# Kernel optimization log

Hardware: AMD Instinct MI355X
Metric: run time of the kernel (lower is better)

Reference implementation:

```python
import jax, jax.numpy as jnp
import numpy as np


def bilinear_sample(img, xs, ys):
    # img: [C,H,W]; xs, ys: [Ho,Wo] fractional source coords (pixel units).
    # Zero-fill outside the image, matching grid_sample(padding_mode='zeros').
    C, H, W = img.shape
    x0f = jnp.floor(xs); y0f = jnp.floor(ys)
    wx = xs - x0f; wy = ys - y0f
    x0 = x0f.astype(jnp.int32); y0 = y0f.astype(jnp.int32)

    def gather(yi, xi):
        inb = ((xi >= 0) & (xi <= W - 1) & (yi >= 0) & (yi <= H - 1))
        xc = jnp.clip(xi, 0, W - 1); yc = jnp.clip(yi, 0, H - 1)
        return img[:, yc, xc] * inb[None].astype(img.dtype)

    v00 = gather(y0,     x0)
    v01 = gather(y0,     x0 + 1)
    v10 = gather(y0 + 1, x0)
    v11 = gather(y0 + 1, x0 + 1)
    return (v00 * (1 - wx) * (1 - wy) + v01 * wx * (1 - wy)
            + v10 * (1 - wx) * wy + v11 * wx * wy)


def setup_inputs() -> dict:
    key = jax.random.key(0)
    k1, k2 = jax.random.split(key)
    frame = jax.random.uniform(k1, (1, 4, 1080, 1920), dtype=jnp.float32)
    # last channel is the alpha/transparency mask: fully opaque frame
    frame = frame.at[:, -1].set(1.0)
    canvas = jax.random.uniform(k2, (1, 4, 2048, 3072), dtype=jnp.float32)
    # realistic near-identity homography: small rotation + translation + tiny perspective
    th = 0.02
    Hmat = jnp.array([[np.cos(th), -np.sin(th), 400.0],
                      [np.sin(th),  np.cos(th), 300.0],
                      [1e-6,        0.0,        1.0]], dtype=jnp.float32)
    return {"frame": frame, "Hmat": Hmat, "canvas": canvas}


def reference(frame, Hmat, canvas):
    # Homography warp of `frame` into the canvas coordinate grid (inverse warp +
    # bilinear resample), then 'over' alpha-compositing onto the canvas
    # (merge_frame), fused into one pass over the canvas buffer.
    _, C, Hc, Wc = canvas.shape
    Hinv = jnp.linalg.inv(Hmat)
    dt = frame.dtype
    ys, xs = jnp.meshgrid(jnp.arange(Hc, dtype=dt), jnp.arange(Wc, dtype=dt), indexing='ij')
    coords = jnp.stack([xs, ys, jnp.ones_like(xs)])          # [3,Hc,Wc]
    src = jnp.einsum('ij,jhw->ihw', Hinv, coords)            # [3,Hc,Wc]
    sx = src[0] / src[2]
    sy = src[1] / src[2]
    warped = bilinear_sample(frame[0], sx, sy)               # [C,Hc,Wc]
    a_s = warped[-1:]                                        # source alpha
    a_c = canvas[0, -1:]                                     # canvas alpha
    out_rgb = warped[:-1] * a_s + canvas[0, :-1] * a_c * (1.0 - a_s)
    out_a = a_s + a_c * (1.0 - a_s)
    return jnp.concatenate([out_rgb, out_a], axis=0)[None]   # [1,C,Hc,Wc]
```

## Files before the change

kernel.cpp:

```cpp
#include <hip/hip_runtime.h>


#define FH 1080
#define FW 1920
#define CHh 2048
#define CWw 3072
#define FHW (FH * FW)
#define CHW (CHh * CWw)

__global__ __launch_bounds__(256) void interleave_kernel(
    const float* __restrict__ frame, float4* __restrict__ fi)
{
    const int idx = blockIdx.x * 256 + threadIdx.x;
    float4 v;
    v.x = frame[idx];
    v.y = frame[FHW + idx];
    v.z = frame[2 * FHW + idx];
    v.w = frame[3 * FHW + idx];
    fi[idx] = v;
}

__global__ __launch_bounds__(256) void pano1_kernel(
    const float4* __restrict__ fi,
    const float* __restrict__ Hm,
    const float* __restrict__ canvas,
    float* __restrict__ out)
{
    const int x = blockIdx.x * 256 + threadIdx.x;
    const int y = blockIdx.y;
    const int pix = y * CWw + x;

    const float a  = Hm[0], b  = Hm[1], c  = Hm[2];
    const float d  = Hm[3], e  = Hm[4], f  = Hm[5];
    const float g  = Hm[6], hh = Hm[7], i9 = Hm[8];
    const float A0 = e * i9 - f * hh, A1 = c * hh - b * i9, A2 = b * f - c * e;
    const float B0 = f * g  - d * i9, B1 = a * i9 - c * g,  B2 = c * d - a * f;
    const float C0 = d * hh - e * g,  C1 = b * g  - a * hh, C2 = a * e - b * d;

    const float xf = (float)x, yf = (float)y;
    const float u = fmaf(A0, xf, fmaf(A1, yf, A2));
    const float v = fmaf(B0, xf, fmaf(B1, yf, B2));
    const float w = fmaf(C0, xf, fmaf(C1, yf, C2));
    const float invw = __builtin_amdgcn_rcpf(w);
    const float sx = u * invw;
    const float sy = v * invw;

    const float x0f = floorf(sx);
    const float y0f = floorf(sy);
    const float wx = sx - x0f;
    const float wy = sy - y0f;
    const int x0 = (int)x0f;
    const int y0 = (int)y0f;

    const float c0 = canvas[0 * CHW + pix];
    const float c1 = canvas[1 * CHW + pix];
    const float c2 = canvas[2 * CHW + pix];
    const float ac = canvas[3 * CHW + pix];

    float wr = 0.f, wg = 0.f, wb = 0.f, wa = 0.f;

    if (x0 >= -1 && x0 <= FW - 1 && y0 >= -1 && y0 <= FH - 1) {
        const int x1 = x0 + 1, y1 = y0 + 1;
        const float mx0 = (x0 >= 0) ? 1.f : 0.f;
        const float mx1 = (x1 <= FW - 1) ? 1.f : 0.f;
        const float my0 = (y0 >= 0) ? 1.f : 0.f;
        const float my1 = (y1 <= FH - 1) ? 1.f : 0.f;
        const int xc0 = min(max(x0, 0), FW - 1);
        const int xc1 = min(max(x1, 0), FW - 1);
        const int yc0 = min(max(y0, 0), FH - 1);
        const int yc1 = min(max(y1, 0), FH - 1);

        const float w00 = (1.f - wx) * (1.f - wy) * mx0 * my0;
        const float w01 = wx * (1.f - wy) * mx1 * my0;
        const float w10 = (1.f - wx) * wy * mx0 * my1;
        const float w11 = wx * wy * mx1 * my1;

        const float4 v00 = fi[yc0 * FW + xc0];
        const float4 v01 = fi[yc0 * FW + xc1];
        const float4 v10 = fi[yc1 * FW + xc0];
        const float4 v11 = fi[yc1 * FW + xc1];

        wr = fmaf(w00, v00.x, fmaf(w01, v01.x, fmaf(w10, v10.x, w11 * v11.x)));
        wg = fmaf(w00, v00.y, fmaf(w01, v01.y, fmaf(w10, v10.y, w11 * v11.y)));
        wb = fmaf(w00, v00.z, fmaf(w01, v01.z, fmaf(w10, v10.z, w11 * v11.z)));
        wa = fmaf(w00, v00.w, fmaf(w01, v01.w, fmaf(w10, v10.w, w11 * v11.w)));
    }

    const float k = ac * (1.f - wa);
    out[0 * CHW + pix] = fmaf(wr, wa, c0 * k);
    out[1 * CHW + pix] = fmaf(wg, wa, c1 * k);
    out[2 * CHW + pix] = fmaf(wb, wa, c2 * k);
    out[3 * CHW + pix] = wa + k;
}

__global__ __launch_bounds__(256) void pano_kernel(
    const float* __restrict__ frame,
    const float* __restrict__ Hm,
    const float* __restrict__ canvas,
    float* __restrict__ out)
{
    const int x = blockIdx.x * 256 + threadIdx.x;
    const int y = blockIdx.y;
    const int pix = y * CWw + x;

    const float a  = Hm[0], b  = Hm[1], c  = Hm[2];
    const float d  = Hm[3], e  = Hm[4], f  = Hm[5];
    const float g  = Hm[6], hh = Hm[7], i9 = Hm[8];
    const float A0 = e * i9 - f * hh, A1 = c * hh - b * i9, A2 = b * f - c * e;
    const float B0 = f * g  - d * i9, B1 = a * i9 - c * g,  B2 = c * d - a * f;
    const float C0 = d * hh - e * g,  C1 = b * g  - a * hh, C2 = a * e - b * d;

    const float xf = (float)x, yf = (float)y;
    const float u = A0 * xf + A1 * yf + A2;
    const float v = B0 * xf + B1 * yf + B2;
    const float w = C0 * xf + C1 * yf + C2;
    const float sx = u / w;
    const float sy = v / w;

    const float x0f = floorf(sx);
    const float y0f = floorf(sy);
    const float wx = sx - x0f;
    const float wy = sy - y0f;
    const int x0 = (int)x0f;
    const int y0 = (int)y0f;

    const float c0 = canvas[0 * CHW + pix];
    const float c1 = canvas[1 * CHW + pix];
    const float c2 = canvas[2 * CHW + pix];
    const float ac = canvas[3 * CHW + pix];

    float w0 = 0.f, w1 = 0.f, w2 = 0.f, as = 0.f;
    if (x0 >= -1 && x0 <= FW - 1 && y0 >= -1 && y0 <= FH - 1) {
        const int x1 = x0 + 1, y1 = y0 + 1;
        const float mx0 = (x0 >= 0) ? 1.f : 0.f;
        const float mx1 = (x1 <= FW - 1) ? 1.f : 0.f;
        const float my0 = (y0 >= 0) ? 1.f : 0.f;
        const float my1 = (y1 <= FH - 1) ? 1.f : 0.f;
        const int xc0 = min(max(x0, 0), FW - 1);
        const int xc1 = min(max(x1, 0), FW - 1);
        const int yc0 = min(max(y0, 0), FH - 1);
        const int yc1 = min(max(y1, 0), FH - 1);

        const float w00 = (1.f - wx) * (1.f - wy) * mx0 * my0;
        const float w01 = wx * (1.f - wy) * mx1 * my0;
        const float w10 = (1.f - wx) * wy * mx0 * my1;
        const float w11 = wx * wy * mx1 * my1;

        const int i00 = yc0 * FW + xc0;
        const int i01 = yc0 * FW + xc1;
        const int i10 = yc1 * FW + xc0;
        const int i11 = yc1 * FW + xc1;

        #pragma unroll
        for (int chn = 0; chn < 4; ++chn) {
            const float* fp = frame + chn * FHW;
            const float val = w00 * fp[i00] + w01 * fp[i01]
                            + w10 * fp[i10] + w11 * fp[i11];
            if (chn == 0) w0 = val;
            else if (chn == 1) w1 = val;
            else if (chn == 2) w2 = val;
            else as = val;
        }
    }

    const float k = ac * (1.f - as);
    out[0 * CHW + pix] = w0 * as + c0 * k;
    out[1 * CHW + pix] = w1 * as + c1 * k;
    out[2 * CHW + pix] = w2 * as + c2 * k;
    out[3 * CHW + pix] = as + k;
}

extern "C" void kernel_launch(void* const* d_in, const int* in_sizes, int n_in,
                              void* d_out, int out_size, void* d_ws, size_t ws_size,
                              hipStream_t stream) {
    const float* frame  = (const float*)d_in[0];
    const float* Hm     = (const float*)d_in[1];
    const float* canvas = (const float*)d_in[2];
    float* out = (float*)d_out;

    const size_t need = (size_t)FHW * sizeof(float4);
    if (ws_size >= need) {
        float4* fi = (float4*)d_ws;
        interleave_kernel<<<dim3(FHW / 256), dim3(256), 0, stream>>>(frame, fi);
        pano1_kernel<<<dim3(CWw / 256, CHh), dim3(256), 0, stream>>>(fi, Hm, canvas, out);
    } else {
        pano_kernel<<<dim3(CWw / 256, CHh), dim3(256), 0, stream>>>(frame, Hm, canvas, out);
    }
}
```

Baseline: 207.1 us.

## Pack frame to fp16 and process two canvas pixels per thread

Replaces the float4 interleaved frame with a half-precision RGBA packed layout, fetching both horizontal bilinear neighbours with one 16-byte load per row. The main kernel now handles two adjacent canvas pixels per thread using float2 loads and stores. This shrinks the workspace and gather traffic and lowers per-pixel instruction overhead, at the cost of fp16 rounding of the source frame values.

```diff
diff --git a/kernel.cpp b/kernel.cpp
--- a/kernel.cpp
+++ b/kernel.cpp
@@ -1,4 +1,5 @@
 #include <hip/hip_runtime.h>
+#include <hip/hip_fp16.h>
 
 
 #define FH 1080
@@ -8,27 +9,42 @@
 #define FHW (FH * FW)
 #define CHW (CHh * CWw)
 
-__global__ __launch_bounds__(256) void interleave_kernel(
-    const float* __restrict__ frame, float4* __restrict__ fi)
+__device__ __forceinline__ unsigned pack2(float a, float b) {
+    union { __half2 h; unsigned u; } c;
+    c.h = __floats2half2_rn(a, b);
+    return c.u;
+}
+__device__ __forceinline__ float2 unpack2(unsigned u) {
+    union { unsigned u; __half2 h; } c;
+    c.u = u;
+    return __half22float2(c.h);
+}
+
+__global__ __launch_bounds__(256) void pack_kernel(
+    const float* __restrict__ frame, uint2* __restrict__ fi)
 {
     const int idx = blockIdx.x * 256 + threadIdx.x;
-    float4 v;
-    v.x = frame[idx];
-    v.y = frame[FHW + idx];
-    v.z = frame[2 * FHW + idx];
-    v.w = frame[3 * FHW + idx];
-    fi[idx] = v;
-}
-
-__global__ __launch_bounds__(256) void pano1_kernel(
-    const float4* __restrict__ fi,
+    uint2 u;
+    u.x = pack2(frame[idx],           frame[FHW + idx]);
+    u.y = pack2(frame[2 * FHW + idx], frame[3 * FHW + idx]);
+    fi[idx] = u;
+}
+
+__global__ __launch_bounds__(256) void pano2_kernel(
+    const uint2* __restrict__ fi,
     const float* __restrict__ Hm,
     const float* __restrict__ canvas,
     float* __restrict__ out)
 {
-    const int x = blockIdx.x * 256 + threadIdx.x;
-    const int y = blockIdx.y;
-    const int pix = y * CWw + x;
+    const int xp = blockIdx.x * 256 + threadIdx.x;
+    const int y  = blockIdx.y;
+    const int q  = y * (CWw / 2) + xp;
+
+    const float2* cv = (const float2*)canvas;
+    const float2 cr = cv[0 * (CHW / 2) + q];
+    const float2 cg = cv[1 * (CHW / 2) + q];
+    const float2 cb = cv[2 * (CHW / 2) + q];
+    const float2 ca = cv[3 * (CHW / 2) + q];
 
     const float a  = Hm[0], b  = Hm[1], c  = Hm[2];
     const float d  = Hm[3], e  = Hm[4], f  = Hm[5];
@@ -37,60 +53,79 @@
     const float B0 = f * g  - d * i9, B1 = a * i9 - c * g,  B2 = c * d - a * f;
     const float C0 = d * hh - e * g,  C1 = b * g  - a * hh, C2 = a * e - b * d;
 
-    const float xf = (float)x, yf = (float)y;
-    const float u = fmaf(A0, xf, fmaf(A1, yf, A2));
-    const float v = fmaf(B0, xf, fmaf(B1, yf, B2));
-    const float w = fmaf(C0, xf, fmaf(C1, yf, C2));
-    const float invw = __builtin_amdgcn_rcpf(w);
-    const float sx = u * invw;
-    const float sy = v * invw;
-
-    const float x0f = floorf(sx);
-    const float y0f = floorf(sy);
-    const float wx = sx - x0f;
-    const float wy = sy - y0f;
-    const int x0 = (int)x0f;
-    const int y0 = (int)y0f;
-
-    const float c0 = canvas[0 * CHW + pix];
-    const float c1 = canvas[1 * CHW + pix];
-    const float c2 = canvas[2 * CHW + pix];
-    const float ac = canvas[3 * CHW + pix];
-
-    float wr = 0.f, wg = 0.f, wb = 0.f, wa = 0.f;
-
-    if (x0 >= -1 && x0 <= FW - 1 && y0 >= -1 && y0 <= FH - 1) {
-        const int x1 = x0 + 1, y1 = y0 + 1;
-        const float mx0 = (x0 >= 0) ? 1.f : 0.f;
-        const float mx1 = (x1 <= FW - 1) ? 1.f : 0.f;
-        const float my0 = (y0 >= 0) ? 1.f : 0.f;
-        const float my1 = (y1 <= FH - 1) ? 1.f : 0.f;
-        const int xc0 = min(max(x0, 0), FW - 1);
-        const int xc1 = min(max(x1, 0), FW - 1);
-        const int yc0 = min(max(y0, 0), FH - 1);
-        const int yc1 = min(max(y1, 0), FH - 1);
-
-        const float w00 = (1.f - wx) * (1.f - wy) * mx0 * my0;
-        const float w01 = wx * (1.f - wy) * mx1 * my0;
-        const float w10 = (1.f - wx) * wy * mx0 * my1;
-        const float w11 = wx * wy * mx1 * my1;
-
-        const float4 v00 = fi[yc0 * FW + xc0];
-        const float4 v01 = fi[yc0 * FW + xc1];
-        const float4 v10 = fi[yc1 * FW + xc0];
-        const float4 v11 = fi[yc1 * FW + xc1];
-
-        wr = fmaf(w00, v00.x, fmaf(w01, v01.x, fmaf(w10, v10.x, w11 * v11.x)));
-        wg = fmaf(w00, v00.y, fmaf(w01, v01.y, fmaf(w10, v10.y, w11 * v11.y)));
-        wb = fmaf(w00, v00.z, fmaf(w01, v01.z, fmaf(w10, v10.z, w11 * v11.z)));
-        wa = fmaf(w00, v00.w, fmaf(w01, v01.w, fmaf(w10, v10.w, w11 * v11.w)));
-    }
-
-    const float k = ac * (1.f - wa);
-    out[0 * CHW + pix] = fmaf(wr, wa, c0 * k);
-    out[1 * CHW + pix] = fmaf(wg, wa, c1 * k);
-    out[2 * CHW + pix] = fmaf(wb, wa, c2 * k);
-    out[3 * CHW + pix] = wa + k;
+    float wr[2], wg[2], wb[2], wa[2];
+    const float yf = (float)y;
+
+    #pragma unroll
+    for (int p = 0; p < 2; ++p) {
+        wr[p] = wg[p] = wb[p] = wa[p] = 0.f;
+        const float xf = (float)(2 * xp + p);
+        const float u = fmaf(A0, xf, fmaf(A1, yf, A2));
+        const float v = fmaf(B0, xf, fmaf(B1, yf, B2));
+        const float w = fmaf(C0, xf, fmaf(C1, yf, C2));
+        const float invw = __builtin_amdgcn_rcpf(w);
+        const float sx = u * invw;
+        const float sy = v * invw;
+
+        const float x0f = floorf(sx);
+        const float y0f = floorf(sy);
+        const float wx = sx - x0f;
+        const float wy = sy - y0f;
+        const int x0 = (int)x0f;
+        const int y0 = (int)y0f;
+
+        if (x0 >= -1 && x0 <= FW - 1 && y0 >= -1 && y0 <= FH - 1) {
+            const int y1 = y0 + 1;
+            const float mx0 = (x0 >= 0) ? 1.f : 0.f;
+            const float mx1 = (x0 + 1 <= FW - 1) ? 1.f : 0.f;
+            const float my0 = (y0 >= 0) ? 1.f : 0.f;
+            const float my1 = (y1 <= FH - 1) ? 1.f : 0.f;
+
+            const int bse = min(max(x0, 0), FW - 2);
+            const bool sel = (x0 == bse);
+            const int yc0 = min(max(y0, 0), FH - 1);
+            const int yc1 = min(max(y1, 0), FH - 1);
+
+            const uint4 r0 = *(const uint4*)((const char*)fi + (size_t)(yc0 * FW + bse) * 8u);
+            const uint4 r1 = *(const uint4*)((const char*)fi + (size_t)(yc1 * FW + bse) * 8u);
+
+            const unsigned u00a = sel ? r0.x : r0.z, u00b = sel ? r0.y : r0.w;
+            const unsigned u01a = sel ? r0.z : r0.x, u01b = sel ? r0.w : r0.y;
+            const unsigned u10a = sel ? r1.x : r1.z, u10b = sel ? r1.y : r1.w;
+            const unsigned u11a = sel ? r1.z : r1.x, u11b = sel ? r1.w : r1.y;
+
+            const float2 v00rg = unpack2(u00a), v00ba = unpack2(u00b);
+            const float2 v01rg = unpack2(u01a), v01ba = unpack2(u01b);
+            const float2 v10rg = unpack2(u10a), v10ba = unpack2(u10b);
+            const float2 v11rg = unpack2(u11a), v11ba = unpack2(u11b);
+
+            const float w00 = (1.f - wx) * (1.f - wy) * mx0 * my0;
+            const float w01 = wx * (1.f - wy) * mx1 * my0;
+            const float w10 = (1.f - wx) * wy * mx0 * my1;
+            const float w11 = wx * wy * mx1 * my1;
+
+            wr[p] = fmaf(w00, v00rg.x, fmaf(w01, v01rg.x, fmaf(w10, v10rg.x, w11 * v11rg.x)));
+            wg[p] = fmaf(w00, v00rg.y, fmaf(w01, v01rg.y, fmaf(w10, v10rg.y, w11 * v11rg.y)));
+            wb[p] = fmaf(w00, v00ba.x, fmaf(w01, v01ba.x, fmaf(w10, v10ba.x, w11 * v11ba.x)));
+            wa[p] = fmaf(w00, v00ba.y, fmaf(w01, v01ba.y, fmaf(w10, v10ba.y, w11 * v11ba.y)));
+        }
+    }
+
+    float2 o0, o1, o2, o3;
+    {
+        const float k0 = ca.x * (1.f - wa[0]);
+        const float k1 = ca.y * (1.f - wa[1]);
+        o0 = make_float2(fmaf(wr[0], wa[0], cr.x * k0), fmaf(wr[1], wa[1], cr.y * k1));
+        o1 = make_float2(fmaf(wg[0], wa[0], cg.x * k0), fmaf(wg[1], wa[1], cg.y * k1));
+        o2 = make_float2(fmaf(wb[0], wa[0], cb.x * k0), fmaf(wb[1], wa[1], cb.y * k1));
+        o3 = make_float2(wa[0] + k0, wa[1] + k1);
+    }
+
+    float2* ov = (float2*)out;
+    ov[0 * (CHW / 2) + q] = o0;
+    ov[1 * (CHW / 2) + q] = o1;
+    ov[2 * (CHW / 2) + q] = o2;
+    ov[3 * (CHW / 2) + q] = o3;
 }
 
 __global__ __launch_bounds__(256) void pano_kernel(
@@ -178,11 +213,11 @@
     const float* canvas = (const float*)d_in[2];
     float* out = (float*)d_out;
 
-    const size_t need = (size_t)FHW * sizeof(float4);
+    const size_t need = (size_t)FHW * sizeof(uint2);
     if (ws_size >= need) {
-        float4* fi = (float4*)d_ws;
-        interleave_kernel<<<dim3(FHW / 256), dim3(256), 0, stream>>>(frame, fi);
-        pano1_kernel<<<dim3(CWw / 256, CHh), dim3(256), 0, stream>>>(fi, Hm, canvas, out);
+        uint2* fi = (uint2*)d_ws;
+        pack_kernel<<<dim3(FHW / 256), dim3(256), 0, stream>>>(frame, fi);
+        pano2_kernel<<<dim3(CWw / 2 / 256, CHh), dim3(256), 0, stream>>>(fi, Hm, canvas, out);
     } else {
         pano_kernel<<<dim3(CWw / 256, CHh), dim3(256), 0, stream>>>(frame, Hm, canvas, out);
     }
```

Result: no change. 209.2 us (+1.0%).
